# Optimization experiments

Measured on AMD Instinct MI355X. Metric: run time of the kernel, lower is better.

## Reference

```python
import jax, jax.numpy as jnp
import numpy as np

B, T, V, EMB, KBD, H, NF, OUT = 256, 50, 100000, 64, 64, 128, 10, 64


def setup_inputs() -> dict:
    key = jax.random.key(0)
    ks = jax.random.split(key, 18)
    s = 0.05
    f = lambda i, shape: jax.random.normal(ks[i], shape, jnp.float32) * s
    return {
        "X": jax.random.randint(ks[0], (B, T), 0, V),
        "E": f(1, (V, EMB)),
        "KBE": f(2, (V, KBD)),
        "r_matrix": f(3, (NF, KBD)),
        "gru_Wih": f(4, (3 * H, EMB)),
        "gru_Whh": f(5, (3 * H, H)),
        "gru_bih": f(6, (3 * H,)),
        "gru_bhh": f(7, (3 * H,)),
        "u_W": f(8, (KBD, H)),
        "u_b": f(9, (KBD,)),
        "ea_W": f(10, (KBD, KBD)),
        "ea_b": f(11, (KBD,)),
        "u2_W": f(12, (H, KBD + H)),
        "u2_b": f(13, (H,)),
        "m1_W": f(14, (OUT, H)),
        "m1_b": f(15, (OUT,)),
        "m2_W": f(16, (OUT, EMB + KBD)),
        "m2_b": f(17, (OUT,)),
    }


def reference(X, E, KBE, r_matrix, gru_Wih, gru_Whh, gru_bih, gru_bhh,
              u_W, u_b, ea_W, ea_b, u2_W, u2_b, m1_W, m1_b, m2_W, m2_b):
    b, t = X.shape
    nf, d = r_matrix.shape
    hdim = gru_Whh.shape[1]
    # mask row 0 of the embedding tables (padding item)
    Em = E.at[0].set(0.0)
    KBEm = KBE.at[0].set(0.0)
    Sx = Em[X]        # [B,T,EMB]
    KBx = KBEm[X]     # [B,T,KBD]

    h0 = jnp.zeros((b, hdim), Sx.dtype)
    MN0 = jnp.zeros((b, nf, d), Sx.dtype)
    ysum0 = jnp.zeros((b, m1_b.shape[0]), Sx.dtype)

    def step(carry, xs):
        h, MN, ysum = carry
        x_emb, kb = xs
        # torch GRUCell
        gi = x_emb @ gru_Wih.T + gru_bih
        gh = h @ gru_Whh.T + gru_bhh
        ir, iz, inn = jnp.split(gi, 3, axis=1)
        hr, hz, hn = jnp.split(gh, 3, axis=1)
        r = jax.nn.sigmoid(ir + hr)
        z = jax.nn.sigmoid(iz + hz)
        n = jnp.tanh(inn + r * hn)
        h = (1.0 - z) * n + z * h
        # memory write
        EA = jnp.tanh(kb @ ea_W.T + ea_b)[:, None, :] + r_matrix      # [B,NF,D]
        gate = jax.nn.sigmoid(jnp.sum(MN * EA, axis=-1, keepdims=True))  # [B,NF,1]
        MN = MN * (1.0 - gate) + EA * gate
        # memory read
        U = jnp.tanh(h @ u_W.T + u_b)                                  # [B,D]
        AW = jax.nn.softmax(U @ r_matrix.T, axis=1)                    # [B,NF]
        AC = jnp.einsum('bnd,bn->bd', MN, AW)                          # [B,D]
        Ut = jnp.tanh(jnp.concatenate([h, AC], axis=-1) @ u2_W.T + u2_b)
        y = jnp.tanh(Ut @ m1_W.T + m1_b)                               # [B,OUT]
        return (h, MN, ysum + y), None

    (h, MN, ysum), _ = jax.lax.scan(
        step, (h0, MN0, ysum0),
        (Sx.transpose(1, 0, 2), KBx.transpose(1, 0, 2)))
    y = ysum / t

    MergeE = jnp.concatenate([E, KBE], axis=1).at[0].set(0.0)  # [V, EMB+KBD]
    Sy = jnp.tanh(MergeE @ m2_W.T + m2_b)                      # [V, OUT]
    return jax.nn.log_softmax(y @ Sy.T, axis=1)                # [B, V]
```

## Files before the change

kernel.cpp:

```cpp
#include <hip/hip_runtime.h>
#include <hip/hip_bf16.h>
#include <math.h>

#define BB 256
#define TT 50
#define VV 100000
#define EMB 64
#define KBD 64
#define HH 128
#define NF 10
#define OUTD 64
#define G3H 384
#define NTILE 6250
#define DSTR 16
#define NSY 240

typedef __attribute__((ext_vector_type(8))) short sh8;
typedef __attribute__((ext_vector_type(4))) short sh4;
typedef __attribute__((ext_vector_type(4))) float f32x4;

__device__ __forceinline__ float frcp(float x){ return __builtin_amdgcn_rcpf(x); }
__device__ __forceinline__ float sigm(float x){ return frcp(1.0f+__expf(-x)); }
__device__ __forceinline__ float tanhf_(float x){ return 1.0f - 2.0f*frcp(__expf(2.0f*x)+1.0f); }
__device__ __forceinline__ short f2bs(float f){ __hip_bfloat16 h=__float2bfloat16(f); return *reinterpret_cast<short*>(&h); }
__device__ __forceinline__ sh8 ldfrag(const float* p){
  float4 a = *(const float4*)p; float4 b = *(const float4*)(p+4);
  sh8 v;
  v[0]=f2bs(a.x); v[1]=f2bs(a.y); v[2]=f2bs(a.z); v[3]=f2bs(a.w);
  v[4]=f2bs(b.x); v[5]=f2bs(b.y); v[6]=f2bs(b.z); v[7]=f2bs(b.w);
  return v;
}
__device__ __forceinline__ void barrier_lds(){
  asm volatile("s_waitcnt lgkmcnt(0)" ::: "memory");
  __builtin_amdgcn_sched_barrier(0);
  __builtin_amdgcn_s_barrier();
  __builtin_amdgcn_sched_barrier(0);
}

#define PREP 32
__global__ __launch_bounds__(512) void k_pre(
    const int* __restrict__ X, const float* __restrict__ E, const float* __restrict__ KBE,
    const float* __restrict__ Wih, const float* __restrict__ bih, const float* __restrict__ bhh,
    const float* __restrict__ eaW, const float* __restrict__ eab,
    float* __restrict__ gi_pre, float* __restrict__ ea_pre,
    __hip_bfloat16* __restrict__ ea_bfT, float* __restrict__ denom) {
  const int tid = threadIdx.x;
  const int w = tid>>6, l = tid&63, r16 = l&15, g4 = l>>4;

  if (blockIdx.x == 0){
    for (int i=tid;i<BB*DSTR;i+=512) denom[i]=0.f;
  }
  __shared__ float xeL[PREP][68];
  __shared__ float kbL[PREP][68];
  int base = blockIdx.x * PREP;
  for (int i=tid; i<PREP*EMB; i+=512){
    int p=i>>6, k=i&63; int x = X[base+p];
    xeL[p][k] = x ? E[(size_t)x*EMB+k] : 0.0f;
    kbL[p][k] = x ? KBE[(size_t)x*KBD+k] : 0.0f;
  }
  __syncthreads();

  const int m = w>>2, nq = w&3;
  sh8 axe[2], akb[2];
  #pragma unroll
  for (int f=0;f<2;f++){
    axe[f] = ldfrag(&xeL[m*16 + r16][f*32 + g4*8]);
    akb[f] = ldfrag(&kbL[m*16 + r16][f*32 + g4*8]);
  }
  #pragma unroll
  for (int i=0;i<6;i++){
    int nt = nq*6 + i;
    int j = nt*16 + r16;
    sh8 bf0 = ldfrag(Wih + (size_t)j*EMB + g4*8);
    sh8 bf1 = ldfrag(Wih + (size_t)j*EMB + 32 + g4*8);
    f32x4 acc = {0.f,0.f,0.f,0.f};
    acc = __builtin_amdgcn_mfma_f32_16x16x32_bf16(axe[0], bf0, acc,0,0,0);
    acc = __builtin_amdgcn_mfma_f32_16x16x32_bf16(axe[1], bf1, acc,0,0,0);
    float bj = bih[j] + (j < 2*HH ? bhh[j] : 0.0f);
    #pragma unroll
    for (int r=0;r<4;r++){
      int pair = base + m*16 + g4*4 + r;
      gi_pre[(size_t)pair*G3H + j] = acc[r] + bj;
    }
  }
  {
    int d = nq*16 + r16;
    sh8 bf0 = ldfrag(eaW + (size_t)d*KBD + g4*8);
    sh8 bf1 = ldfrag(eaW + (size_t)d*KBD + 32 + g4*8);
    f32x4 acc = {0.f,0.f,0.f,0.f};
    acc = __builtin_amdgcn_mfma_f32_16x16x32_bf16(akb[0], bf0, acc,0,0,0);
    acc = __builtin_amdgcn_mfma_f32_16x16x32_bf16(akb[1], bf1, acc,0,0,0);
    float bd = eab[d];
    #pragma unroll
    for (int r=0;r<4;r++){
      int pair = base + m*16 + g4*4 + r;
      float v = tanhf(acc[r] + bd);
      ea_pre[(size_t)pair*KBD + d] = v;
      int bb = pair/TT, tt = pair - bb*TT;
      ea_bfT[((size_t)bb*64 + d)*64 + tt] = __float2bfloat16(v);
    }
  }
}

__global__ __launch_bounds__(256,2) void k_scanh(
    const float* __restrict__ gi_pre,
    const float* __restrict__ Whh, const float* __restrict__ bhh,
    const float* __restrict__ ea_pre, const float* __restrict__ rmat,
    float* __restrict__ Gg, float* __restrict__ Pg,
    __hip_bfloat16* __restrict__ h_stream) {
  const int tid = threadIdx.x;
  const int w = tid>>6, l = tid&63, r16 = l&15, g4 = l>>4;

  if (blockIdx.x >= 16) {
    const int b = (blockIdx.x-16)*4 + w;
    sh8 aa[4][2];
    #pragma unroll
    for (int i=0;i<4;i++){
      int row = i*16 + r16; if (row > TT-1) row = TT-1;
      #pragma unroll
      for (int f=0;f<2;f++)
        aa[i][f] = ldfrag(ea_pre + ((size_t)b*TT + row)*KBD + f*32 + g4*8);
    }
    sh8 rmB[2];
    #pragma unroll
    for (int f=0;f<2;f++){
      sh8 z = {0,0,0,0,0,0,0,0};
      if (r16 < NF) z = ldfrag(rmat + (size_t)r16*KBD + f*32 + g4*8);
      rmB[f] = z;
    }
    float* Gb = Gg + ((size_t)b<<12);
    #pragma unroll
    for (int i=0;i<4;i++){
      #pragma unroll
      for (int j=0;j<4;j++){
        f32x4 acc={0.f,0.f,0.f,0.f};
        #pragma unroll
        for (int f=0;f<2;f++) acc = __builtin_amdgcn_mfma_f32_16x16x32_bf16(aa[i][f], aa[j][f], acc,0,0,0);
        #pragma unroll
        for (int r=0;r<4;r++) Gb[(i*16+g4*4+r)*64 + j*16+r16] = acc[r];
      }
      f32x4 accp={0.f,0.f,0.f,0.f};
      #pragma unroll
      for (int f=0;f<2;f++) accp = __builtin_amdgcn_mfma_f32_16x16x32_bf16(aa[i][f], rmB[f], accp,0,0,0);
      #pragma unroll
      for (int r=0;r<4;r++) Pg[((size_t)b<<10) + (i*16+g4*4+r)*16 + r16] = accp[r];
    }
    return;
  }

  __shared__ __hip_bfloat16 hcat[2][16][128];
  __builtin_amdgcn_s_setprio(1);
  const int b = blockIdx.x;
  const int b0 = b*16;
  for (int i=tid;i<2*16*128;i+=256) ((short*)hcat)[i]=0;
  __syncthreads();
  const int swz = (r16&7)<<4;

  sh8 whhF[2][3][4];
  #pragma unroll
  for (int t=0;t<2;t++)
    #pragma unroll
    for (int g=0;g<3;g++){
      int chain = (w + 4*t) + 8*g;
      #pragma unroll
      for (int f=0;f<4;f++)
        whhF[t][g][f] = ldfrag(Whh + (size_t)(chain*16 + r16)*HH + f*32 + g4*8);
    }
  float4 bhn[2];
  bhn[0] = *(const float4*)(bhh + 2*HH + w*16 + g4*4);
  bhn[1] = *(const float4*)(bhh + 2*HH + (w+4)*16 + g4*4);
  float h_old[2][4] = {{0.f,0.f,0.f,0.f},{0.f,0.f,0.f,0.f}};
  const float* gi_row = gi_pre + (size_t)(b0+r16)*TT*G3H;
  __hip_bfloat16* hsb = h_stream + (size_t)b*TT*16*HH;

  int cur = 0;
  auto stepfn = [&](int s, float4 (&gi)[2][3], int cu){
    const char* hrow = (const char*)&hcat[cu][r16][0];
    sh8 hb[4];
    #pragma unroll
    for (int f=0;f<4;f++)
      hb[f] = *(const sh8*)(hrow + ((f*64 + g4*16) ^ swz));
    f32x4 aR[2], aZ[2], aN[2];
    #pragma unroll
    for (int t=0;t<2;t++){ f32x4 z={0.f,0.f,0.f,0.f}; aR[t]=z; aZ[t]=z; aN[t]=z; }
    #pragma unroll
    for (int f=0;f<4;f++){
      #pragma unroll
      for (int t=0;t<2;t++){
        aR[t] = __builtin_amdgcn_mfma_f32_16x16x32_bf16(whhF[t][0][f], hb[f], aR[t],0,0,0);
        aZ[t] = __builtin_amdgcn_mfma_f32_16x16x32_bf16(whhF[t][1][f], hb[f], aZ[t],0,0,0);
        aN[t] = __builtin_amdgcn_mfma_f32_16x16x32_bf16(whhF[t][2][f], hb[f], aN[t],0,0,0);
      }
    }
    char* hwrow = (char*)&hcat[cu^1][r16][0];
    #pragma unroll
    for (int t=0;t<2;t++){
      sh4 hp;
      #pragma unroll
      for (int r=0;r<4;r++){
        float rr = sigm(gi[t][0][r] + aR[t][r]);
        float zz = sigm(gi[t][1][r] + aZ[t][r]);
        float nn = tanhf_(gi[t][2][r] + rr*(aN[t][r] + bhn[t][r]));
        h_old[t][r] = (1.f-zz)*nn + zz*h_old[t][r];
        hp[r] = f2bs(h_old[t][r]);
      }
      *(sh4*)(hwrow + (((w+4*t)*32 + g4*8) ^ swz)) = hp;
      *(sh4*)(hsb + ((size_t)s*16 + r16)*HH + (w+4*t)*16 + g4*4) = hp;
    }
    barrier_lds();
  };

  float4 gA[2][3], gB[2][3];
  #pragma unroll
  for (int t=0;t<2;t++)
    #pragma unroll
    for (int g=0;g<3;g++)
      gA[t][g] = *(const float4*)(gi_row + g*128 + (w+4*t)*16 + g4*4);

  for (int s=0;s<TT;s+=2){
    {
      int sg = s+1;
      #pragma unroll
      for (int t=0;t<2;t++)
        #pragma unroll
        for (int g=0;g<3;g++)
          gB[t][g] = *(const float4*)(gi_row + (size_t)sg*G3H + g*128 + (w+4*t)*16 + g4*4);
      stepfn(s, gA, cur);
      cur ^= 1;
    }
    {
      int sg = (s+2<TT)? s+2 : TT-1;
      #pragma unroll
      for (int t=0;t<2;t++)
        #pragma unroll
        for (int g=0;g<3;g++)
          gA[t][g] = *(const float4*)(gi_row + (size_t)sg*G3H + g*128 + (w+4*t)*16 + g4*4);
      stepfn(s+1, gB, cur);
      cur ^= 1;
    }
  }
}

__global__ __launch_bounds__(512) void k_uaw(
    const __hip_bfloat16* __restrict__ h_stream,
    const float* __restrict__ uW, const float* __restrict__ ub,
    const float* __restrict__ rmat, float* __restrict__ aw_pre) {
  __shared__ __hip_bfloat16 u_sh[8][16][72];
  const int tid = threadIdx.x;
  const int w = tid>>6, l = tid&63, r16 = l&15, g4 = l>>4;
  sh8 uwF[4][4];
  #pragma unroll
  for (int ot=0;ot<4;ot++)
    #pragma unroll
    for (int f=0;f<4;f++)
      uwF[ot][f] = ldfrag(uW + (size_t)(ot*16+r16)*HH + f*32 + g4*8);
  sh8 rmF[2];
  #pragma unroll
  for (int f=0;f<2;f++){
    sh8 z = {0,0,0,0,0,0,0,0};
    if (r16 < NF) z = ldfrag(rmat + (size_t)r16*KBD + f*32 + g4*8);
    rmF[f] = z;
  }
  float4 ubv[4];
  #pragma unroll
  for (int ot=0;ot<4;ot++) ubv[ot] = *(const float4*)(ub + ot*16 + g4*4);

  int p0 = (blockIdx.x*8 + w)*16;
  int t = p0>>8, b0 = p0&255, fb = b0>>4;
  const __hip_bfloat16* hp = h_stream + (size_t)((fb*TT + t)*16)*HH;
  sh8 hb[4];
  #pragma unroll
  for (int f=0;f<4;f++) hb[f] = *(const sh8*)(hp + r16*HH + f*32 + g4*8);
  f32x4 u[4];
  #pragma unroll
  for (int ot=0;ot<4;ot++){ f32x4 z={0.f,0.f,0.f,0.f}; u[ot]=z; }
  #pragma unroll
  for (int ot=0;ot<4;ot++)
    #pragma unroll
    for (int f=0;f<4;f++)
      u[ot] = __builtin_amdgcn_mfma_f32_16x16x32_bf16(uwF[ot][f], hb[f], u[ot],0,0,0);
  #pragma unroll
  for (int ot=0;ot<4;ot++){
    sh4 up;
    #pragma unroll
    for (int r=0;r<4;r++) up[r] = f2bs(tanhf_(u[ot][r] + ubv[ot][r]));
    *(sh4*)&u_sh[w][l&15][ot*16 + g4*4] = up;
  }
  __syncthreads();
  sh8 uf[2];
  #pragma unroll
  for (int f=0;f<2;f++) uf[f] = *(const sh8*)&u_sh[w][r16][f*32 + g4*8];
  f32x4 al={0.f,0.f,0.f,0.f};
  #pragma unroll
  for (int f=0;f<2;f++) al = __builtin_amdgcn_mfma_f32_16x16x32_bf16(rmF[f], uf[f], al,0,0,0);
  float mx = -1e30f;
  #pragma unroll
  for (int r=0;r<4;r++){ if (g4*4+r < NF) mx = fmaxf(mx, al[r]); }
  mx = fmaxf(mx, __shfl_xor(mx,16));
  mx = fmaxf(mx, __shfl_xor(mx,32));
  float av[4]; float ssum=0.f;
  #pragma unroll
  for (int r=0;r<4;r++){ av[r] = (g4*4+r < NF) ? __expf(al[r]-mx) : 0.f; ssum += av[r]; }
  ssum += __shfl_xor(ssum,16); ssum += __shfl_xor(ssum,32);
  float inv = frcp(ssum);
  if (g4<3){
    f32x4 o = {av[0]*inv, av[1]*inv, av[2]*inv, av[3]*inv};
    *(f32x4*)&aw_pre[(size_t)(p0+r16)*16 + g4*4] = o;
  }
}

__global__ __launch_bounds__(640) void k_mnac(
    const float* __restrict__ Gg, const float* __restrict__ Pg,
    const float* __restrict__ rmat, const float* __restrict__ aw_pre,
    const __hip_bfloat16* __restrict__ ea_bfT,
    __hip_bfloat16* __restrict__ ac_pre) {
  __shared__ float AagL[64*52];
  __shared__ float BagL[64*16];
  const int tid = threadIdx.x;
  const int n = tid>>6, l = tid&63;
  const int b = blockIdx.x;
  for (int i=tid;i<64*52;i+=640) AagL[i]=0.f;
  for (int i=tid;i<64*16;i+=640) BagL[i]=0.f;

  float rv = rmat[n*KBD + l];
  float R = rv*rv;
  R += __shfl_xor(R,1); R += __shfl_xor(R,2); R += __shfl_xor(R,4);
  R += __shfl_xor(R,8); R += __shfl_xor(R,16); R += __shfl_xor(R,32);

  float Pn = (l<TT)? Pg[((size_t)b<<10) + l*16 + n] : 0.f;
  const float* Gb = Gg + ((size_t)b<<12);
  float Grow = Gb[l];
  float awt = aw_pre[(size_t)(0*256+b)*16 + n];
  float d=0.f, w_=0.f, q=1.f;
  __syncthreads();

  for (int t=0;t<TT;t++){
    int tn = (t+1<TT)? t+1 : TT-1;
    float GrowN = Gb[tn*64 + l];
    float awtN  = aw_pre[(size_t)(tn*256+b)*16 + n];
    float dt = __shfl(d, t);
    float g  = sigm(dt);
    float og = 1.f - g;
    float Pt = __shfl(Pn, t);
    float Ets = Grow + Pt + Pn + R;
    d = og*d + g*Ets;
    w_ = (l==t)? g : w_*og;
    q *= og;
    if (l < TT) atomicAdd(&AagL[t*52 + l], awt*w_);
    if (l == 0) BagL[t*16 + n] = awt*(1.f - q);
    Grow = GrowN; awt = awtN;
  }
  __syncthreads();

  const int w = n, r16 = l&15, g4 = l>>4;
  if (w < 4){
    sh8 a1[4][2], a2[4];
    #pragma unroll
    for (int i=0;i<4;i++){
      int row = i*16 + r16;
      #pragma unroll
      for (int f=0;f<2;f++) a1[i][f] = ldfrag(&AagL[row*52 + f*32 + g4*8]);
      a2[i] = ldfrag(&BagL[row*16 + ((g4*8) & 15)]);
      if (g4 >= 2){ sh8 z={0,0,0,0,0,0,0,0}; a2[i]=z; }
    }
    int j = w;
    sh8 bb1[2];
    #pragma unroll
    for (int f=0;f<2;f++)
      bb1[f] = *(const sh8*)(ea_bfT + ((size_t)b<<12) + (j*16+r16)*64 + f*32 + g4*8);
    sh8 bb2;
    #pragma unroll
    for (int c=0;c<8;c++){
      int k = g4*8 + c;
      bb2[c] = (k<NF)? f2bs(rmat[k*KBD + j*16+r16]) : (short)0;
    }
    #pragma unroll
    for (int i=0;i<4;i++){
      f32x4 acc={0.f,0.f,0.f,0.f};
      #pragma unroll
      for (int f=0;f<2;f++) acc = __builtin_amdgcn_mfma_f32_16x16x32_bf16(a1[i][f], bb1[f], acc,0,0,0);
      acc = __builtin_amdgcn_mfma_f32_16x16x32_bf16(a2[i], bb2, acc,0,0,0);
      #pragma unroll
      for (int r=0;r<4;r++){
        int t = i*16 + g4*4 + r;
        if (t < TT)
          ac_pre[((size_t)t*256 + b)*KBD + j*16 + r16] = __float2bfloat16(acc[r]);
      }
    }
  }
}

__global__ __launch_bounds__(512) void k_uty(
    const __hip_bfloat16* __restrict__ h_stream, const __hip_bfloat16* __restrict__ ac_pre,
    const float* __restrict__ u2W, const float* __restrict__ u2b,
    const float* __restrict__ m1W, const float* __restrict__ m1b,
    __hip_bfloat16* __restrict__ y_tmp,
    const float* __restrict__ E, const float* __restrict__ KBE,
    const float* __restrict__ m2W, const float* __restrict__ m2b,
    __hip_bfloat16* __restrict__ Sy) {
  __shared__ __hip_bfloat16 ut_sh[16][136];
  const int tid = threadIdx.x;
  const int w = tid>>6, l = tid&63, r16 = l&15, g4 = l>>4;

  if (blockIdx.x >= 800) {
    int kof = g4*8;
    sh8 bbf[4][4];
    float bias[4];
    #pragma unroll
    for (int nt=0;nt<4;nt++){
      int o = nt*16 + r16;
      bias[nt] = m2b[o];
      #pragma unroll
      for (int ks=0;ks<4;ks++) bbf[nt][ks] = ldfrag(m2W + o*128 + ks*32 + kof);
    }
    int wid = (blockIdx.x-800)*8 + w;
    for (int tile=wid; tile<NTILE; tile+=NSY*8){
      int v = tile*16 + r16;
      sh8 aa[4];
      const float* ep = E + (size_t)v*EMB + kof;
      const float* kp = KBE + (size_t)v*KBD + kof;
      aa[0] = ldfrag(ep); aa[1] = ldfrag(ep+32);
      aa[2] = ldfrag(kp); aa[3] = ldfrag(kp+32);
      if (v==0){ sh8 z={0,0,0,0,0,0,0,0}; aa[0]=z;aa[1]=z;aa[2]=z;aa[3]=z; }
      f32x4 acc[4];
      #pragma unroll
      for (int nt=0;nt<4;nt++){ f32x4 z={0.f,0.f,0.f,0.f}; acc[nt]=z; }
      #pragma unroll
      for (int nt=0;nt<4;nt++)
        #pragma unroll
        for (int ks=0;ks<4;ks++)
          acc[nt] = __builtin_amdgcn_mfma_f32_16x16x32_bf16(aa[ks],bbf[nt][ks],acc[nt],0,0,0);
      #pragma unroll
      for (int nt=0;nt<4;nt++){
        #pragma unroll
        for (int r=0;r<4;r++){
          int vv = tile*16 + g4*4 + r;
          Sy[(size_t)vv*OUTD + nt*16 + r16] = __float2bfloat16(tanhf_(acc[nt][r] + bias[nt]));
        }
      }
    }
    return;
  }

  const int t = blockIdx.x>>4, btile = blockIdx.x&15;
  const int b0 = btile*16, fb = btile;

  sh8 u2F[6];
  #pragma unroll
  for (int f=0;f<6;f++) u2F[f] = ldfrag(u2W + (size_t)(w*16+r16)*(HH+KBD) + f*32 + g4*8);
  sh8 m1F[4];
  if (w<4){
    #pragma unroll
    for (int f=0;f<4;f++) m1F[f] = ldfrag(m1W + (size_t)(w*16+r16)*HH + f*32 + g4*8);
  }
  float4 u2bv = *(const float4*)(u2b + w*16 + g4*4);

  const __hip_bfloat16* hp = h_stream + (size_t)((fb*TT + t)*16)*HH;
  const __hip_bfloat16* ap = ac_pre + ((size_t)t*256 + b0)*KBD;
  sh8 cb[6];
  #pragma unroll
  for (int f=0;f<4;f++) cb[f] = *(const sh8*)(hp + r16*HH + f*32 + g4*8);
  #pragma unroll
  for (int f=4;f<6;f++) cb[f] = *(const sh8*)(ap + r16*KBD + (f-4)*32 + g4*8);
  f32x4 at={0.f,0.f,0.f,0.f};
  #pragma unroll
  for (int f=0;f<6;f++) at = __builtin_amdgcn_mfma_f32_16x16x32_bf16(u2F[f], cb[f], at,0,0,0);
  sh4 tp;
  #pragma unroll
  for (int r=0;r<4;r++) tp[r] = f2bs(tanhf_(at[r] + u2bv[r]));
  *(sh4*)&ut_sh[r16][w*16+g4*4] = tp;
  __syncthreads();
  if (w<4){
    float4 m1bv = *(const float4*)(m1b + w*16 + g4*4);
    sh8 tb[4];
    #pragma unroll
    for (int f=0;f<4;f++) tb[f] = *(const sh8*)&ut_sh[r16][f*32+g4*8];
    f32x4 ay={0.f,0.f,0.f,0.f};
    #pragma unroll
    for (int f=0;f<4;f++) ay = __builtin_amdgcn_mfma_f32_16x16x32_bf16(m1F[f], tb[f], ay,0,0,0);
    sh4 yp;
    #pragma unroll
    for (int r=0;r<4;r++) yp[r] = f2bs(tanhf_(ay[r] + m1bv[r]));
    *(sh4*)&y_tmp[((size_t)t*256 + b0 + r16)*OUTD + w*16 + g4*4] = yp;
  }
}

__global__ __launch_bounds__(512) void k_fin(
    const __hip_bfloat16* __restrict__ y_tmp, __hip_bfloat16* __restrict__ ybf) {
  int idx = blockIdx.x*512 + threadIdx.x;
  int b = idx>>6, o = idx&63;
  float s = 0.f;
  for (int t=0;t<TT;t++) s += __bfloat162float(y_tmp[((size_t)t*256 + b)*OUTD + o]);
  ybf[(size_t)b*OUTD + o] = __float2bfloat16(s*(1.0f/TT));
}

__global__ __launch_bounds__(256) void k_logits(
    const __hip_bfloat16* __restrict__ ybf, const __hip_bfloat16* __restrict__ Sy,
    float* __restrict__ denom, float* __restrict__ out, int pass) {
  __shared__ float dsum[64];
  int lane = threadIdx.x & 63;
  int w = threadIdx.x >> 6;
  int r16 = lane & 15, g4 = lane >> 4;
  int kof = g4 * 8;
  int tbase = blockIdx.x * 16 + w * 4;
  if (pass==0){
    if (threadIdx.x<64) dsum[threadIdx.x]=0.f;
    __syncthreads();
  }
  sh8 b0[4], b1[4];
  #pragma unroll
  for (int i=0;i<4;i++){
    if (tbase + i < NTILE) {
      const __hip_bfloat16* bp = Sy + ((size_t)((tbase+i)*16 + r16))*OUTD + kof;
      b0[i] = *(const sh8*)bp;
      b1[i] = *(const sh8*)(bp + 32);
    } else {
      sh8 z = {0,0,0,0,0,0,0,0};
      b0[i]=z; b1[i]=z;
    }
  }
  int bg0 = blockIdx.y * 4;
  for (int bgi=0; bgi<4; bgi++){
    int bg = bg0 + bgi;
    const __hip_bfloat16* ap = ybf + (bg*16 + r16)*OUTD + kof;
    sh8 a0 = *(const sh8*)ap;
    sh8 a1 = *(const sh8*)(ap+32);
    if (pass == 0){
      float part[4] = {0.f,0.f,0.f,0.f};
      #pragma unroll
      for (int i=0;i<4;i++){
        if (tbase + i < NTILE){
          f32x4 acc = {0.f,0.f,0.f,0.f};
          acc = __builtin_amdgcn_mfma_f32_16x16x32_bf16(a0,b0[i],acc,0,0,0);
          acc = __builtin_amdgcn_mfma_f32_16x16x32_bf16(a1,b1[i],acc,0,0,0);
          #pragma unroll
          for (int r=0;r<4;r++) part[r] += __expf(acc[r]);
        }
      }
      #pragma unroll
      for (int r=0;r<4;r++){
        float p = part[r];
        p += __shfl_xor(p,1,16); p += __shfl_xor(p,2,16);
        p += __shfl_xor(p,4,16); p += __shfl_xor(p,8,16);
        if (r16==0) atomicAdd(&dsum[bgi*16 + g4*4 + r], p);
      }
    } else {
      float lse[4];
      #pragma unroll
      for (int r=0;r<4;r++) lse[r] = logf(denom[(size_t)(bg*16 + g4*4 + r)*DSTR]);
      #pragma unroll
      for (int i=0;i<4;i++){
        if (tbase + i < NTILE){
          f32x4 acc = {0.f,0.f,0.f,0.f};
          acc = __builtin_amdgcn_mfma_f32_16x16x32_bf16(a0,b0[i],acc,0,0,0);
          acc = __builtin_amdgcn_mfma_f32_16x16x32_bf16(a1,b1[i],acc,0,0,0);
          int vc = (tbase+i)*16 + r16;
          #pragma unroll
          for (int r=0;r<4;r++)
            out[(size_t)(bg*16 + g4*4 + r)*VV + vc] = acc[r] - lse[r];
        }
      }
    }
  }
  if (pass==0){
    __syncthreads();
    if (threadIdx.x<64)
      atomicAdd(&denom[(size_t)(bg0*16 + threadIdx.x)*DSTR], dsum[threadIdx.x]);
  }
}

extern "C" void kernel_launch(void* const* d_in, const int* in_sizes, int n_in,
                              void* d_out, int out_size, void* d_ws, size_t ws_size,
                              hipStream_t stream) {
  const int*   X    = (const int*)  d_in[0];
  const float* E    = (const float*)d_in[1];
  const float* KBE  = (const float*)d_in[2];
  const float* rmat = (const float*)d_in[3];
  const float* Wih  = (const float*)d_in[4];
  const float* Whh  = (const float*)d_in[5];
  const float* bih  = (const float*)d_in[6];
  const float* bhh  = (const float*)d_in[7];
  const float* uW   = (const float*)d_in[8];
  const float* ub   = (const float*)d_in[9];
  const float* eaW  = (const float*)d_in[10];
  const float* eab  = (const float*)d_in[11];
  const float* u2W  = (const float*)d_in[12];
  const float* u2b  = (const float*)d_in[13];
  const float* m1W  = (const float*)d_in[14];
  const float* m1b  = (const float*)d_in[15];
  const float* m2W  = (const float*)d_in[16];
  const float* m2b  = (const float*)d_in[17];
  float* outp = (float*)d_out;

  char* p = (char*)d_ws;
  float* gi_pre = (float*)p;            p += (size_t)BB*TT*G3H*4;
  float* ea_pre = (float*)p;            p += (size_t)BB*TT*KBD*4;
  float* denom  = (float*)p;            p += (size_t)BB*DSTR*4;
  float* aw_pre = (float*)p;            p += (size_t)BB*TT*16*4;
  float* Gg     = (float*)p;            p += (size_t)BB*64*64*4;
  float* Pg     = (float*)p;            p += (size_t)BB*64*16*4;
  __hip_bfloat16* h_stream = (__hip_bfloat16*)p; p += (size_t)16*TT*16*HH*2;
  __hip_bfloat16* ea_bfT = (__hip_bfloat16*)p;   p += (size_t)BB*64*64*2;
  __hip_bfloat16* ac_pre = (__hip_bfloat16*)p;   p += (size_t)BB*TT*KBD*2;
  __hip_bfloat16* y_tmp  = (__hip_bfloat16*)p;   p += (size_t)BB*TT*OUTD*2;
  __hip_bfloat16* ybf    = (__hip_bfloat16*)p;   p += (size_t)BB*OUTD*2;
  __hip_bfloat16* Sy     = (__hip_bfloat16*)p;   p += (size_t)VV*OUTD*2;

  k_pre<<<400,512,0,stream>>>(X,E,KBE,Wih,bih,bhh,eaW,eab,gi_pre,ea_pre,ea_bfT,denom);
  k_scanh<<<80,256,0,stream>>>(gi_pre,Whh,bhh,ea_pre,rmat,Gg,Pg,h_stream);
  k_uaw<<<100,512,0,stream>>>(h_stream,uW,ub,rmat,aw_pre);
  k_mnac<<<256,640,0,stream>>>(Gg,Pg,rmat,aw_pre,ea_bfT,ac_pre);
  k_uty<<<800+NSY,512,0,stream>>>(h_stream,ac_pre,u2W,u2b,m1W,m1b,y_tmp,
                                  E,KBE,m2W,m2b,Sy);
  k_fin<<<32,512,0,stream>>>(y_tmp,ybf);
  dim3 g1((NTILE + 15)/16, 4, 1);
  k_logits<<<g1,256,0,stream>>>(ybf,Sy,denom,outp,0);
  k_logits<<<g1,256,0,stream>>>(ybf,Sy,denom,outp,1);
}
```

Before: 227.9 us.

## Fuse attention-weight kernel into memory kernel and atomically accumulate y sum

The U/softmax attention-weight computation moves from its own kernel into the start of k_mnac. Each block computes its batch row's 50 timesteps in shared memory, so the aw_pre round trip through global memory goes away. The y time-averaging kernel is also dropped: k_uty atomically adds tanh outputs into an fp32 buffer, which k_logits scales by 1/T while building its bf16 fragments. This removes two launches and intermediate traffic, in exchange for redundant uW fragment loads per block and many global atomics on a small buffer.

```diff
diff --git a/kernel.cpp b/kernel.cpp
--- a/kernel.cpp
+++ b/kernel.cpp
@@ -30,6 +30,13 @@
   v[4]=f2bs(b.x); v[5]=f2bs(b.y); v[6]=f2bs(b.z); v[7]=f2bs(b.w);
   return v;
 }
+__device__ __forceinline__ sh8 ldfrag_s(const float* p, float s){
+  float4 a = *(const float4*)p; float4 b = *(const float4*)(p+4);
+  sh8 v;
+  v[0]=f2bs(a.x*s); v[1]=f2bs(a.y*s); v[2]=f2bs(a.z*s); v[3]=f2bs(a.w*s);
+  v[4]=f2bs(b.x*s); v[5]=f2bs(b.y*s); v[6]=f2bs(b.z*s); v[7]=f2bs(b.w*s);
+  return v;
+}
 __device__ __forceinline__ void barrier_lds(){
   asm volatile("s_waitcnt lgkmcnt(0)" ::: "memory");
   __builtin_amdgcn_sched_barrier(0);
@@ -43,12 +50,14 @@
     const float* __restrict__ Wih, const float* __restrict__ bih, const float* __restrict__ bhh,
     const float* __restrict__ eaW, const float* __restrict__ eab,
     float* __restrict__ gi_pre, float* __restrict__ ea_pre,
-    __hip_bfloat16* __restrict__ ea_bfT, float* __restrict__ denom) {
+    __hip_bfloat16* __restrict__ ea_bfT, float* __restrict__ denom,
+    float* __restrict__ ybf32) {
   const int tid = threadIdx.x;
   const int w = tid>>6, l = tid&63, r16 = l&15, g4 = l>>4;
 
   if (blockIdx.x == 0){
     for (int i=tid;i<BB*DSTR;i+=512) denom[i]=0.f;
+    for (int i=tid;i<BB*OUTD;i+=512) ybf32[i]=0.f;
   }
   __shared__ float xeL[PREP][68];
   __shared__ float kbL[PREP][68];
@@ -241,86 +250,79 @@
   }
 }
 
-__global__ __launch_bounds__(512) void k_uaw(
+__global__ __launch_bounds__(640) void k_mnac(
+    const float* __restrict__ Gg, const float* __restrict__ Pg,
+    const float* __restrict__ rmat,
     const __hip_bfloat16* __restrict__ h_stream,
     const float* __restrict__ uW, const float* __restrict__ ub,
-    const float* __restrict__ rmat, float* __restrict__ aw_pre) {
-  __shared__ __hip_bfloat16 u_sh[8][16][72];
-  const int tid = threadIdx.x;
-  const int w = tid>>6, l = tid&63, r16 = l&15, g4 = l>>4;
-  sh8 uwF[4][4];
-  #pragma unroll
-  for (int ot=0;ot<4;ot++)
-    #pragma unroll
-    for (int f=0;f<4;f++)
-      uwF[ot][f] = ldfrag(uW + (size_t)(ot*16+r16)*HH + f*32 + g4*8);
-  sh8 rmF[2];
-  #pragma unroll
-  for (int f=0;f<2;f++){
-    sh8 z = {0,0,0,0,0,0,0,0};
-    if (r16 < NF) z = ldfrag(rmat + (size_t)r16*KBD + f*32 + g4*8);
-    rmF[f] = z;
-  }
-  float4 ubv[4];
-  #pragma unroll
-  for (int ot=0;ot<4;ot++) ubv[ot] = *(const float4*)(ub + ot*16 + g4*4);
-
-  int p0 = (blockIdx.x*8 + w)*16;
-  int t = p0>>8, b0 = p0&255, fb = b0>>4;
-  const __hip_bfloat16* hp = h_stream + (size_t)((fb*TT + t)*16)*HH;
-  sh8 hb[4];
-  #pragma unroll
-  for (int f=0;f<4;f++) hb[f] = *(const sh8*)(hp + r16*HH + f*32 + g4*8);
-  f32x4 u[4];
-  #pragma unroll
-  for (int ot=0;ot<4;ot++){ f32x4 z={0.f,0.f,0.f,0.f}; u[ot]=z; }
-  #pragma unroll
-  for (int ot=0;ot<4;ot++)
-    #pragma unroll
-    for (int f=0;f<4;f++)
-      u[ot] = __builtin_amdgcn_mfma_f32_16x16x32_bf16(uwF[ot][f], hb[f], u[ot],0,0,0);
-  #pragma unroll
-  for (int ot=0;ot<4;ot++){
-    sh4 up;
-    #pragma unroll
-    for (int r=0;r<4;r++) up[r] = f2bs(tanhf_(u[ot][r] + ubv[ot][r]));
-    *(sh4*)&u_sh[w][l&15][ot*16 + g4*4] = up;
-  }
-  __syncthreads();
-  sh8 uf[2];
-  #pragma unroll
-  for (int f=0;f<2;f++) uf[f] = *(const sh8*)&u_sh[w][r16][f*32 + g4*8];
-  f32x4 al={0.f,0.f,0.f,0.f};
-  #pragma unroll
-  for (int f=0;f<2;f++) al = __builtin_amdgcn_mfma_f32_16x16x32_bf16(rmF[f], uf[f], al,0,0,0);
-  float mx = -1e30f;
-  #pragma unroll
-  for (int r=0;r<4;r++){ if (g4*4+r < NF) mx = fmaxf(mx, al[r]); }
-  mx = fmaxf(mx, __shfl_xor(mx,16));
-  mx = fmaxf(mx, __shfl_xor(mx,32));
-  float av[4]; float ssum=0.f;
-  #pragma unroll
-  for (int r=0;r<4;r++){ av[r] = (g4*4+r < NF) ? __expf(al[r]-mx) : 0.f; ssum += av[r]; }
-  ssum += __shfl_xor(ssum,16); ssum += __shfl_xor(ssum,32);
-  float inv = frcp(ssum);
-  if (g4<3){
-    f32x4 o = {av[0]*inv, av[1]*inv, av[2]*inv, av[3]*inv};
-    *(f32x4*)&aw_pre[(size_t)(p0+r16)*16 + g4*4] = o;
-  }
-}
-
-__global__ __launch_bounds__(640) void k_mnac(
-    const float* __restrict__ Gg, const float* __restrict__ Pg,
-    const float* __restrict__ rmat, const float* __restrict__ aw_pre,
     const __hip_bfloat16* __restrict__ ea_bfT,
     __hip_bfloat16* __restrict__ ac_pre) {
+  __shared__ __hip_bfloat16 U_sh[64][72];
+  __shared__ float aw_sh[64*16];
   __shared__ float AagL[64*52];
   __shared__ float BagL[64*16];
   const int tid = threadIdx.x;
-  const int n = tid>>6, l = tid&63;
+  const int n = tid>>6, l = tid&63, r16 = l&15, g4 = l>>4;
   const int b = blockIdx.x;
   for (int i=tid;i<64*52;i+=640) AagL[i]=0.f;
   for (int i=tid;i<64*16;i+=640) BagL[i]=0.f;
+
+  const __hip_bfloat16* hsb = h_stream + ((size_t)(b>>4)*TT)*16*HH + (size_t)(b&15)*HH;
+
+  #pragma unroll
+  for (int cc=0; cc<2; cc++){
+    int c = n + cc*10;
+    if (c < 16){
+      int mi = c>>2, ni = c&3;
+      int t = mi*16 + r16; int tt = (t<TT)? t : TT-1;
+      sh8 hfr[4], wfr[4];
+      #pragma unroll
+      for (int f=0;f<4;f++){
+        hfr[f] = *(const sh8*)(hsb + (size_t)tt*16*HH + f*32 + g4*8);
+        wfr[f] = ldfrag(uW + (size_t)(ni*16+r16)*HH + f*32 + g4*8);
+      }
+      f32x4 acc = {0.f,0.f,0.f,0.f};
+      #pragma unroll
+      for (int f=0;f<4;f++)
+        acc = __builtin_amdgcn_mfma_f32_16x16x32_bf16(wfr[f], hfr[f], acc,0,0,0);
+      float4 ubv = *(const float4*)(ub + ni*16 + g4*4);
+      #pragma unroll
+      for (int r=0;r<4;r++)
+        U_sh[mi*16 + r16][ni*16 + g4*4 + r] = __float2bfloat16(tanhf_(acc[r] + ubv[r]));
+    }
+  }
+  __syncthreads();
+  if (n < 4){
+    sh8 rmF[2];
+    #pragma unroll
+    for (int f=0;f<2;f++){
+      sh8 z = {0,0,0,0,0,0,0,0};
+      if (r16 < NF) z = ldfrag(rmat + (size_t)r16*KBD + f*32 + g4*8);
+      rmF[f] = z;
+    }
+    sh8 uf[2];
+    #pragma unroll
+    for (int f=0;f<2;f++) uf[f] = *(const sh8*)&U_sh[n*16 + r16][f*32 + g4*8];
+    f32x4 al={0.f,0.f,0.f,0.f};
+    #pragma unroll
+    for (int f=0;f<2;f++) al = __builtin_amdgcn_mfma_f32_16x16x32_bf16(rmF[f], uf[f], al,0,0,0);
+    float mx = -1e30f;
+    #pragma unroll
+    for (int r=0;r<4;r++){ if (g4*4+r < NF) mx = fmaxf(mx, al[r]); }
+    mx = fmaxf(mx, __shfl_xor(mx,16));
+    mx = fmaxf(mx, __shfl_xor(mx,32));
+    float av[4]; float ssum=0.f;
+    #pragma unroll
+    for (int r=0;r<4;r++){ av[r] = (g4*4+r < NF) ? __expf(al[r]-mx) : 0.f; ssum += av[r]; }
+    ssum += __shfl_xor(ssum,16); ssum += __shfl_xor(ssum,32);
+    float inv = frcp(ssum);
+    #pragma unroll
+    for (int r=0;r<4;r++){
+      int nn = g4*4+r;
+      if (nn < NF) aw_sh[(n*16 + r16)*16 + nn] = av[r]*inv;
+    }
+  }
+  __syncthreads();
 
   float rv = rmat[n*KBD + l];
   float R = rv*rv;
@@ -330,14 +332,11 @@
   float Pn = (l<TT)? Pg[((size_t)b<<10) + l*16 + n] : 0.f;
   const float* Gb = Gg + ((size_t)b<<12);
   float Grow = Gb[l];
-  float awt = aw_pre[(size_t)(0*256+b)*16 + n];
   float d=0.f, w_=0.f, q=1.f;
-  __syncthreads();
 
   for (int t=0;t<TT;t++){
     int tn = (t+1<TT)? t+1 : TT-1;
     float GrowN = Gb[tn*64 + l];
-    float awtN  = aw_pre[(size_t)(tn*256+b)*16 + n];
     float dt = __shfl(d, t);
     float g  = sigm(dt);
     float og = 1.f - g;
@@ -346,14 +345,15 @@
     d = og*d + g*Ets;
     w_ = (l==t)? g : w_*og;
     q *= og;
+    float awt = aw_sh[t*16 + n];
     if (l < TT) atomicAdd(&AagL[t*52 + l], awt*w_);
     if (l == 0) BagL[t*16 + n] = awt*(1.f - q);
-    Grow = GrowN; awt = awtN;
+    Grow = GrowN;
   }
   __syncthreads();
 
-  const int w = n, r16 = l&15, g4 = l>>4;
-  if (w < 4){
+  if (n < 4){
+    const int w = n;
     sh8 a1[4][2], a2[4];
     #pragma unroll
     for (int i=0;i<4;i++){
@@ -394,7 +394,7 @@
     const __hip_bfloat16* __restrict__ h_stream, const __hip_bfloat16* __restrict__ ac_pre,
     const float* __restrict__ u2W, const float* __restrict__ u2b,
     const float* __restrict__ m1W, const float* __restrict__ m1b,
-    __hip_bfloat16* __restrict__ y_tmp,
+    float* __restrict__ ybf32,
     const float* __restrict__ E, const float* __restrict__ KBE,
     const float* __restrict__ m2W, const float* __restrict__ m2b,
     __hip_bfloat16* __restrict__ Sy) {
@@ -478,24 +478,14 @@
     f32x4 ay={0.f,0.f,0.f,0.f};
     #pragma unroll
     for (int f=0;f<4;f++) ay = __builtin_amdgcn_mfma_f32_16x16x32_bf16(m1F[f], tb[f], ay,0,0,0);
-    sh4 yp;
-    #pragma unroll
-    for (int r=0;r<4;r++) yp[r] = f2bs(tanhf_(ay[r] + m1bv[r]));
-    *(sh4*)&y_tmp[((size_t)t*256 + b0 + r16)*OUTD + w*16 + g4*4] = yp;
-  }
-}
-
-__global__ __launch_bounds__(512) void k_fin(
-    const __hip_bfloat16* __restrict__ y_tmp, __hip_bfloat16* __restrict__ ybf) {
-  int idx = blockIdx.x*512 + threadIdx.x;
-  int b = idx>>6, o = idx&63;
-  float s = 0.f;
-  for (int t=0;t<TT;t++) s += __bfloat162float(y_tmp[((size_t)t*256 + b)*OUTD + o]);
-  ybf[(size_t)b*OUTD + o] = __float2bfloat16(s*(1.0f/TT));
+    #pragma unroll
+    for (int r=0;r<4;r++)
+      atomicAdd(&ybf32[(size_t)(b0 + r16)*OUTD + w*16 + g4*4 + r], tanhf_(ay[r] + m1bv[r]));
+  }
 }
 
 __global__ __launch_bounds__(256) void k_logits(
-    const __hip_bfloat16* __restrict__ ybf, const __hip_bfloat16* __restrict__ Sy,
+    const float* __restrict__ ybf32, const __hip_bfloat16* __restrict__ Sy,
     float* __restrict__ denom, float* __restrict__ out, int pass) {
   __shared__ float dsum[64];
   int lane = threadIdx.x & 63;
@@ -503,6 +493,7 @@
   int r16 = lane & 15, g4 = lane >> 4;
   int kof = g4 * 8;
   int tbase = blockIdx.x * 16 + w * 4;
+  const float SC = 1.0f/TT;
   if (pass==0){
     if (threadIdx.x<64) dsum[threadIdx.x]=0.f;
     __syncthreads();
@@ -522,9 +513,9 @@
   int bg0 = blockIdx.y * 4;
   for (int bgi=0; bgi<4; bgi++){
     int bg = bg0 + bgi;
-    const __hip_bfloat16* ap = ybf + (bg*16 + r16)*OUTD + kof;
-    sh8 a0 = *(const sh8*)ap;
-    sh8 a1 = *(const sh8*)(ap+32);
+    const float* ap = ybf32 + (size_t)(bg*16 + r16)*OUTD + kof;
+    sh8 a0 = ldfrag_s(ap, SC);
+    sh8 a1 = ldfrag_s(ap+32, SC);
     if (pass == 0){
       float part[4] = {0.f,0.f,0.f,0.f};
       #pragma unroll
@@ -596,24 +587,20 @@
   float* gi_pre = (float*)p;            p += (size_t)BB*TT*G3H*4;
   float* ea_pre = (float*)p;            p += (size_t)BB*TT*KBD*4;
   float* denom  = (float*)p;            p += (size_t)BB*DSTR*4;
-  float* aw_pre = (float*)p;            p += (size_t)BB*TT*16*4;
+  float* ybf32  = (float*)p;            p += (size_t)BB*OUTD*4;
   float* Gg     = (float*)p;            p += (size_t)BB*64*64*4;
   float* Pg     = (float*)p;            p += (size_t)BB*64*16*4;
   __hip_bfloat16* h_stream = (__hip_bfloat16*)p; p += (size_t)16*TT*16*HH*2;
   __hip_bfloat16* ea_bfT = (__hip_bfloat16*)p;   p += (size_t)BB*64*64*2;
   __hip_bfloat16* ac_pre = (__hip_bfloat16*)p;   p += (size_t)BB*TT*KBD*2;
-  __hip_bfloat16* y_tmp  = (__hip_bfloat16*)p;   p += (size_t)BB*TT*OUTD*2;
-  __hip_bfloat16* ybf    = (__hip_bfloat16*)p;   p += (size_t)BB*OUTD*2;
   __hip_bfloat16* Sy     = (__hip_bfloat16*)p;   p += (size_t)VV*OUTD*2;
 
-  k_pre<<<400,512,0,stream>>>(X,E,KBE,Wih,bih,bhh,eaW,eab,gi_pre,ea_pre,ea_bfT,denom);
+  k_pre<<<400,512,0,stream>>>(X,E,KBE,Wih,bih,bhh,eaW,eab,gi_pre,ea_pre,ea_bfT,denom,ybf32);
   k_scanh<<<80,256,0,stream>>>(gi_pre,Whh,bhh,ea_pre,rmat,Gg,Pg,h_stream);
-  k_uaw<<<100,512,0,stream>>>(h_stream,uW,ub,rmat,aw_pre);
-  k_mnac<<<256,640,0,stream>>>(Gg,Pg,rmat,aw_pre,ea_bfT,ac_pre);
-  k_uty<<<800+NSY,512,0,stream>>>(h_stream,ac_pre,u2W,u2b,m1W,m1b,y_tmp,
+  k_mnac<<<256,640,0,stream>>>(Gg,Pg,rmat,h_stream,uW,ub,ea_bfT,ac_pre);
+  k_uty<<<800+NSY,512,0,stream>>>(h_stream,ac_pre,u2W,u2b,m1W,m1b,ybf32,
                                   E,KBE,m2W,m2b,Sy);
-  k_fin<<<32,512,0,stream>>>(y_tmp,ybf);
   dim3 g1((NTILE + 15)/16, 4, 1);
-  k_logits<<<g1,256,0,stream>>>(ybf,Sy,denom,outp,0);
-  k_logits<<<g1,256,0,stream>>>(ybf,Sy,denom,outp,1);
-}
+  k_logits<<<g1,256,0,stream>>>(ybf32,Sy,denom,outp,0);
+  k_logits<<<g1,256,0,stream>>>(ybf32,Sy,denom,outp,1);
+}
```

Result: slower. 233.5 us (+2.5%).
